# Optimization experiments

Hardware: AMD Instinct MI355X
Metric: run time of the kernel (lower is better)

Reference implementation:

```python
import jax, jax.numpy as jnp
import numpy as np


def _bce_logits(x, t):
    # numerically stable BCE-with-logits, elementwise
    return jnp.maximum(x, 0.0) - x * t + jnp.log1p(jnp.exp(-jnp.abs(x)))


def setup_inputs() -> dict:
    key = jax.random.key(0)
    k1, k2, k3, k4, k5 = jax.random.split(key, 5)
    B, A, H, W, C, N = 32, 3, 64, 64, 80, 2048
    pred = jax.random.normal(k1, (B, A, H, W, 5 + C), dtype=jnp.float32)
    tb = jax.random.randint(k2, (N, 1), 0, B).astype(jnp.float32)
    tl = jax.random.randint(k3, (N, 1), 0, C).astype(jnp.float32)
    txy = jax.random.uniform(k4, (N, 2), dtype=jnp.float32)
    twh = jax.random.uniform(k5, (N, 2), minval=0.02, maxval=0.98, dtype=jnp.float32)
    target = jnp.concatenate([tb, tl, txy, twh], axis=-1)  # [N,6]
    anchors = jnp.array([[10.0, 13.0], [33.0, 23.0], [62.0, 45.0]], dtype=jnp.float32)
    return {"pred": pred, "target": target, "anchors": anchors, "num_classes": C}


def reference(pred, target, anchors, num_classes):
    B, A, H, W, _ = pred.shape
    N = target.shape[0]
    # scale normalized xywh to grid units (grid size = pred.size(2) = H)
    t = jnp.concatenate([target[..., :2], target[..., 2:] * H], axis=-1)
    pred_bbox_all = pred[..., :4]
    pred_conf = pred[..., 4:5]          # [B,A,H,W,1]
    pred_cls_all = pred[..., 5:]
    b_idx = t[..., 0].astype(jnp.int32)
    labels = t[..., 1].astype(jnp.int32)
    target_xy = t[..., 2:4]
    target_wh = t[..., 4:6]
    w_idx = target_wh[..., 0].astype(jnp.int32)
    h_idx = target_wh[..., 1].astype(jnp.int32)
    # IoU of same-center (w,h) boxes: [A,N]
    inter = jnp.minimum(anchors[:, None, 0], target_wh[None, :, 0]) * \
            jnp.minimum(anchors[:, None, 1], target_wh[None, :, 1])
    area_a = (anchors[:, 0] * anchors[:, 1])[:, None]
    area_t = (target_wh[:, 0] * target_wh[:, 1])[None, :]
    ious = inter / (area_a + area_t - inter)
    iou_idx = jnp.argmax(ious, axis=0)  # [N]
    txy_frac = target_xy - jnp.floor(target_xy)
    twh_log = jnp.log(target_wh / anchors[iou_idx])
    target_bbox = jnp.concatenate([txy_frac, twh_log], axis=-1)  # [N,4]
    pred_bbox = pred_bbox_all[b_idx, iou_idx, h_idx, w_idx]      # [N,4]
    pred_cls = pred_cls_all[b_idx, iou_idx, h_idx, w_idx]        # [N,C]
    target_cls = jax.nn.one_hot(labels, num_classes, dtype=pred_cls.dtype)
    # obj / noobj masks over [B,A,H,W,1]
    obj = jnp.zeros((B, A, H, W), dtype=pred.dtype).at[b_idx, iou_idx, h_idx, w_idx].set(1.0)
    noobj = 1.0 - obj
    # zero noobj at (batch[i], a, h[i], w[i]) for every anchor a with iou > 0.5
    keep = (ious <= 0.5).astype(pred.dtype)                      # [A,N]
    a_grid = jnp.broadcast_to(jnp.arange(A)[:, None], (A, N))
    b_grid = jnp.broadcast_to(b_idx[None, :], (A, N))
    h_grid = jnp.broadcast_to(h_idx[None, :], (A, N))
    w_grid = jnp.broadcast_to(w_idx[None, :], (A, N))
    noobj = noobj.at[b_grid, a_grid, h_grid, w_grid].mul(keep)
    pc = pred_conf[..., 0]
    n_obj = jnp.sum(obj)
    n_noobj = jnp.sum(noobj)
    conf_sum = jnp.sum(obj * _bce_logits(pc, 1.0)) + jnp.sum(noobj * _bce_logits(pc, 0.0))
    loss_conf = conf_sum / (n_obj + n_noobj)
    loss_xywh = jnp.mean((pred_bbox - target_bbox) ** 2)
    loss_cls = jnp.mean(_bce_logits(pred_cls, target_cls))
    return loss_xywh + loss_conf + loss_cls
```

## Files before the change

kernel.cpp:

```cpp
#include <hip/hip_runtime.h>
#include <math.h>

#define BB 32
#define AA 3
#define HH 64
#define WW 64
#define CC 80
#define NN 2048
#define CH (5 + CC)
#define NCELL (BB * AA * HH * WW)

#define TGT_GRID 8
#define CELL_BLOCKS 768
#define CPT 2
#define CELL_STRIDE (CELL_BLOCKS * 256)
#define TOTAL_BLOCKS (TGT_GRID + CELL_BLOCKS)

#define OBJ_BIT 1u
#define SUP_BIT 4u

__device__ __forceinline__ float bce_pos(float x) {
    return fmaxf(x, 0.f) - x + log1pf(expf(-fabsf(x)));
}
__device__ __forceinline__ float bce_neg(float x) {
    return fmaxf(x, 0.f) + log1pf(expf(-fabsf(x)));
}

__device__ __forceinline__ float wave_reduce(float v) {
    #pragma unroll
    for (int off = 32; off > 0; off >>= 1) v += __shfl_down(v, off, 64);
    return v;
}


__global__ void yolo_mega(const float* __restrict__ pred,
                          const float* __restrict__ target,
                          const float* __restrict__ anchors,
                          unsigned int* __restrict__ mask,
                          float* __restrict__ partial) {
    __shared__ float s_red[4][5];
    int wave = threadIdx.x >> 6, lane = threadIdx.x & 63;
    float cs = 0.f, dob = 0.f, dno = 0.f, lx = 0.f, lc = 0.f;

    if (blockIdx.x < TGT_GRID) {
        int n = blockIdx.x * 256 + threadIdx.x;
        float tx = target[n * 6 + 2] * (float)HH;
        float ty = target[n * 6 + 3] * (float)HH;
        float tw = target[n * 6 + 4] * (float)HH;
        float th = target[n * 6 + 5] * (float)HH;
        int b     = (int)target[n * 6 + 0];
        int label = (int)target[n * 6 + 1];
        int wi = (int)tw;
        int hi = (int)th;

        float area_t = tw * th;
        float ious[AA];
        float best = -1.f;
        int bi = 0;
        #pragma unroll
        for (int a = 0; a < AA; a++) {
            float aw = anchors[a * 2 + 0];
            float ah = anchors[a * 2 + 1];
            float inter = fminf(aw, tw) * fminf(ah, th);
            float iou = inter / (aw * ah + area_t - inter);
            ious[a] = iou;
            if (iou > best) { best = iou; bi = a; }
        }

        #pragma unroll
        for (int a = 0; a < AA; a++) {
            unsigned int bits = 0u;
            if (a == bi) bits |= OBJ_BIT;
            if (ious[a] > 0.5f) bits |= SUP_BIT;
            if (bits) {
                int cell = ((b * AA + a) * HH + hi) * WW + wi;
                unsigned int old = atomicOr(&mask[cell], bits) & (OBJ_BIT | SUP_BIT);
                unsigned int nw = old | bits;
                if (nw != old) {
                    float x = pred[(long)cell * CH + 4];
                    float neg = bce_neg(x), pos = bce_pos(x);
                    float fo_c = (old & OBJ_BIT) ? pos : ((old & SUP_BIT) ? 0.f : neg);
                    float fo_o = (old & OBJ_BIT) ? 1.f : 0.f;
                    float fo_n = (old == 0u) ? 1.f : 0.f;
                    float fn_c = (nw & OBJ_BIT) ? pos : ((nw & SUP_BIT) ? 0.f : neg);
                    float fn_o = (nw & OBJ_BIT) ? 1.f : 0.f;
                    float fn_n = 0.f;
                    cs  += fn_c - fo_c;
                    dob += fn_o - fo_o;
                    dno += fn_n - fo_n;
                }
            }
        }

        long pbase = (long)(((b * AA + bi) * HH + hi) * WW + wi) * CH;
        float t0 = tx - floorf(tx);
        float t1 = ty - floorf(ty);
        float t2 = logf(tw / anchors[bi * 2 + 0]);
        float t3 = logf(th / anchors[bi * 2 + 1]);
        float d0 = pred[pbase + 0] - t0;
        float d1 = pred[pbase + 1] - t1;
        float d2 = pred[pbase + 2] - t2;
        float d3 = pred[pbase + 3] - t3;
        lx = d0 * d0 + d1 * d1 + d2 * d2 + d3 * d3;

        #pragma unroll 8
        for (int c = 0; c < CC; c++) {
            float x = pred[pbase + 5 + c];
            lc += (c == label) ? bce_pos(x) : bce_neg(x);
        }
    } else {
        int tid = (blockIdx.x - TGT_GRID) * 256 + threadIdx.x;
        float x[CPT];
        #pragma unroll
        for (int k = 0; k < CPT; k++) {
            int cell = tid + k * CELL_STRIDE;
            x[k] = pred[(long)cell * CH + 4];
        }
        #pragma unroll
        for (int k = 0; k < CPT; k++) cs += bce_neg(x[k]);
    }

    cs  = wave_reduce(cs);
    dob = wave_reduce(dob);
    dno = wave_reduce(dno);
    lx  = wave_reduce(lx);
    lc  = wave_reduce(lc);
    if (lane == 0) {
        s_red[wave][0] = cs; s_red[wave][1] = dob; s_red[wave][2] = dno;
        s_red[wave][3] = lx; s_red[wave][4] = lc;
    }
    __syncthreads();
    if (threadIdx.x < 5) {
        int j = threadIdx.x;
        partial[blockIdx.x * 5 + j] =
            s_red[0][j] + s_red[1][j] + s_red[2][j] + s_red[3][j];
    }
}

__global__ void yolo_finalize(const float* __restrict__ partial,
                              float* __restrict__ out) {
    __shared__ float s_red[4][5];
    int wave = threadIdx.x >> 6, lane = threadIdx.x & 63;
    float v[5] = {0.f, 0.f, 0.f, 0.f, 0.f};
    for (int i = threadIdx.x; i < TOTAL_BLOCKS; i += 256) {
        #pragma unroll
        for (int j = 0; j < 5; j++) v[j] += partial[i * 5 + j];
    }
    #pragma unroll
    for (int j = 0; j < 5; j++) v[j] = wave_reduce(v[j]);
    if (lane == 0) {
        #pragma unroll
        for (int j = 0; j < 5; j++) s_red[wave][j] = v[j];
    }
    __syncthreads();
    if (threadIdx.x == 0) {
        float cs  = s_red[0][0] + s_red[1][0] + s_red[2][0] + s_red[3][0];
        float dob = s_red[0][1] + s_red[1][1] + s_red[2][1] + s_red[3][1];
        float dno = s_red[0][2] + s_red[1][2] + s_red[2][2] + s_red[3][2];
        float lx  = s_red[0][3] + s_red[1][3] + s_red[2][3] + s_red[3][3];
        float lc  = s_red[0][4] + s_red[1][4] + s_red[2][4] + s_red[3][4];
        float n_obj   = dob;
        float n_noobj = (float)NCELL + dno;
        float loss_xywh = lx / ((float)NN * 4.f);
        float loss_cls  = lc / ((float)NN * (float)CC);
        float loss_conf = cs / (n_obj + n_noobj);
        out[0] = loss_xywh + loss_conf + loss_cls;
    }
}

extern "C" void kernel_launch(void* const* d_in, const int* in_sizes, int n_in,
                              void* d_out, int out_size, void* d_ws, size_t ws_size,
                              hipStream_t stream) {
    const float* pred    = (const float*)d_in[0];
    const float* target  = (const float*)d_in[1];
    const float* anchors = (const float*)d_in[2];
    (void)in_sizes; (void)n_in; (void)out_size; (void)ws_size;

    unsigned int* mask = (unsigned int*)d_ws;
    float* partial     = (float*)((char*)d_ws + (size_t)NCELL * 4);


    yolo_mega<<<TOTAL_BLOCKS, 256, 0, stream>>>(pred, target, anchors, mask, partial);
    yolo_finalize<<<1, 256, 0, stream>>>(partial, (float*)d_out);
}
```

Before: 210.1 us.

## Assign one wavefront per target and one thread per cell

Each target is now handled by a whole 64-lane wavefront instead of one thread. Lanes split the anchor mask updates, the four box terms and the 80 class logits, so the long serial loop of scattered loads goes away. The cell pass now uses one thread per cell over many more blocks, and cell blocks are placed before target blocks in the grid. The goal is to remove the long per-thread tail of the original 8 target blocks. The cost is more blocks and more partial sums for the finalize kernel to reduce.

After: 186.4 us. 11.3% less time.

```diff
diff --git a/kernel.cpp b/kernel.cpp
--- a/kernel.cpp
+++ b/kernel.cpp
@@ -10,11 +10,9 @@
 #define CH (5 + CC)
 #define NCELL (BB * AA * HH * WW)
 
-#define TGT_GRID 8
-#define CELL_BLOCKS 768
-#define CPT 2
-#define CELL_STRIDE (CELL_BLOCKS * 256)
-#define TOTAL_BLOCKS (TGT_GRID + CELL_BLOCKS)
+#define CELL_BLOCKS (NCELL / 256)
+#define TGT_BLOCKS  (NN / 4)
+#define TOTAL_BLOCKS (CELL_BLOCKS + TGT_BLOCKS)
 
 #define OBJ_BIT 1u
 #define SUP_BIT 4u
@@ -42,8 +40,13 @@
     int wave = threadIdx.x >> 6, lane = threadIdx.x & 63;
     float cs = 0.f, dob = 0.f, dno = 0.f, lx = 0.f, lc = 0.f;
 
-    if (blockIdx.x < TGT_GRID) {
-        int n = blockIdx.x * 256 + threadIdx.x;
+    if (blockIdx.x < CELL_BLOCKS) {
+        int cell = blockIdx.x * 256 + threadIdx.x;
+        float x = pred[(long)cell * CH + 4];
+        cs = bce_neg(x);
+    } else {
+        int n = (blockIdx.x - CELL_BLOCKS) * 4 + wave;
+
         float tx = target[n * 6 + 2] * (float)HH;
         float ty = target[n * 6 + 3] * (float)HH;
         float tw = target[n * 6 + 4] * (float)HH;
@@ -67,8 +70,8 @@
             if (iou > best) { best = iou; bi = a; }
         }
 
-        #pragma unroll
-        for (int a = 0; a < AA; a++) {
+        if (lane < AA) {
+            int a = lane;
             unsigned int bits = 0u;
             if (a == bi) bits |= OBJ_BIT;
             if (ious[a] > 0.5f) bits |= SUP_BIT;
@@ -80,44 +83,34 @@
                     float x = pred[(long)cell * CH + 4];
                     float neg = bce_neg(x), pos = bce_pos(x);
                     float fo_c = (old & OBJ_BIT) ? pos : ((old & SUP_BIT) ? 0.f : neg);
-                    float fo_o = (old & OBJ_BIT) ? 1.f : 0.f;
-                    float fo_n = (old == 0u) ? 1.f : 0.f;
-                    float fn_c = (nw & OBJ_BIT) ? pos : ((nw & SUP_BIT) ? 0.f : neg);
-                    float fn_o = (nw & OBJ_BIT) ? 1.f : 0.f;
-                    float fn_n = 0.f;
-                    cs  += fn_c - fo_c;
-                    dob += fn_o - fo_o;
-                    dno += fn_n - fo_n;
+                    float fn_c = (nw  & OBJ_BIT) ? pos : ((nw  & SUP_BIT) ? 0.f : neg);
+                    cs  = fn_c - fo_c;
+                    dob = ((nw & OBJ_BIT) ? 1.f : 0.f) - ((old & OBJ_BIT) ? 1.f : 0.f);
+                    dno = -((old == 0u) ? 1.f : 0.f);
                 }
             }
         }
 
         long pbase = (long)(((b * AA + bi) * HH + hi) * WW + wi) * CH;
-        float t0 = tx - floorf(tx);
-        float t1 = ty - floorf(ty);
-        float t2 = logf(tw / anchors[bi * 2 + 0]);
-        float t3 = logf(th / anchors[bi * 2 + 1]);
-        float d0 = pred[pbase + 0] - t0;
-        float d1 = pred[pbase + 1] - t1;
-        float d2 = pred[pbase + 2] - t2;
-        float d3 = pred[pbase + 3] - t3;
-        lx = d0 * d0 + d1 * d1 + d2 * d2 + d3 * d3;
 
-        #pragma unroll 8
-        for (int c = 0; c < CC; c++) {
-            float x = pred[pbase + 5 + c];
-            lc += (c == label) ? bce_pos(x) : bce_neg(x);
+        if (lane < 4) {
+            float t0 = tx - floorf(tx);
+            float t1 = ty - floorf(ty);
+            float t2 = logf(tw / anchors[bi * 2 + 0]);
+            float t3 = logf(th / anchors[bi * 2 + 1]);
+            float tt = (lane == 0) ? t0 : (lane == 1) ? t1 : (lane == 2) ? t2 : t3;
+            float d = pred[pbase + lane] - tt;
+            lx = d * d;
         }
-    } else {
-        int tid = (blockIdx.x - TGT_GRID) * 256 + threadIdx.x;
-        float x[CPT];
-        #pragma unroll
-        for (int k = 0; k < CPT; k++) {
-            int cell = tid + k * CELL_STRIDE;
-            x[k] = pred[(long)cell * CH + 4];
+        {
+            float x = pred[pbase + 5 + lane];
+            lc = (lane == label) ? bce_pos(x) : bce_neg(x);
+            if (lane < CC - 64) {
+                int c2 = 64 + lane;
+                float x2 = pred[pbase + 5 + c2];
+                lc += (c2 == label) ? bce_pos(x2) : bce_neg(x2);
+            }
         }
-        #pragma unroll
-        for (int k = 0; k < CPT; k++) cs += bce_neg(x[k]);
     }
 
     cs  = wave_reduce(cs);
```
